# Performance work log

Measured on AMD Instinct MI355X. Metric: run time of the kernel, lower is better.

## Reference

```python
import jax, jax.numpy as jnp
import numpy as np

M = 2048            # input image is M x M
N_ANGLES = 64       # theta = [0, 1, ..., 63] radians (raw floats, as in the TF layer)

# Daubechies-like 2x2 filters, reshaped row-major exactly like tf.reshape([...,4],[2,2,1,1])
HIGH_F = jnp.array([[-0.1384, 0.7243], [-0.6038, 0.1601]], dtype=jnp.float32)


def setup_inputs() -> dict:
    key = jax.random.key(0)
    image = jax.random.normal(key, (M, M), dtype=jnp.float32)
    return {"image": image}


def _dwt_high(image):
    # tf.nn.conv2d(x, k, strides=2, padding='SAME') with single in/out channel.
    # Input dims are even so SAME adds no padding; out = (H/2, W/2).
    x = image[None, :, :, None]
    k = HIGH_F[:, :, None, None]  # HWIO
    y = jax.lax.conv_general_dilated(
        x, k, window_strides=(2, 2), padding='SAME',
        dimension_numbers=('NHWC', 'HWIO', 'NHWC'))
    return y[0, :, :, 0]


def _pad_square(img):
    # Static (trace-time) padding math, mirrors prepare_img.
    h, w = img.shape
    diagonal = np.sqrt(2) * max(h, w)
    pad = [int(np.ceil(diagonal - s)) for s in (h, w)]
    new_center = [(s + p) // 2 for s, p in zip((h, w), pad)]
    old_center = [s // 2 for s in (h, w)]
    pad_before = [nc - oc for oc, nc in zip(old_center, new_center)]
    pad_width = [(pb, p - pb) for pb, p in zip(pad_before, pad)]
    padded = jnp.pad(img, pad_width, mode='constant', constant_values=0.0)
    center = padded.shape[0] // 2
    return padded, center


def _rotate_sum(img, center, out_h, out_w, angle):
    # ImageProjectiveTransformV3 (BILINEAR, fill_mode=WRAP) followed by sum over rows.
    H, W = img.shape
    xs = jnp.arange(out_w, dtype=jnp.float32)
    ys = jnp.arange(out_h, dtype=jnp.float32)
    X, Y = jnp.meshgrid(xs, ys)  # [out_h, out_w]
    c, s = jnp.cos(angle), jnp.sin(angle)
    x_in = c * X + s * Y - center * (c + s - 1.0)
    y_in = -s * X + c * Y - center * (c - s - 1.0)
    x0 = jnp.floor(x_in)
    y0 = jnp.floor(y_in)
    dx = x_in - x0
    dy = y_in - y0
    # WRAP fill mode: periodic wrapping of sample indices
    x0i = jnp.mod(x0.astype(jnp.int32), W)
    x1i = jnp.mod(x0i + 1, W)
    y0i = jnp.mod(y0.astype(jnp.int32), H)
    y1i = jnp.mod(y0i + 1, H)
    v00 = img[y0i, x0i]
    v01 = img[y0i, x1i]
    v10 = img[y1i, x0i]
    v11 = img[y1i, x1i]
    rotated = (v00 * (1 - dy) * (1 - dx) + v01 * (1 - dy) * dx
               + v10 * dy * (1 - dx) + v11 * dy * dx)
    return rotated.sum(axis=0)  # column sums -> one radon line, length out_w


def reference(image):
    theta = jnp.arange(N_ANGLES, dtype=jnp.float32)  # radians, matches init theta
    high = _dwt_high(image)                          # (1024, 1024)
    padded, center = _pad_square(high)               # (1449, 1449), center 724
    out_h, out_w = padded.shape[0] - 1, padded.shape[1] - 1
    lines = jax.vmap(lambda a: _rotate_sum(padded, center, out_h, out_w, a))(theta)
    A = lines.T                                      # (out_w, n_angles)
    return A / jnp.max(A)
```

## Files before the change

kernel.cpp:

```cpp
#include <hip/hip_runtime.h>
#include <hip/hip_bf16.h>
#include <hip/hip_fp16.h>


#define HM 1024
#define PW 1449
#define PWS 1450
#define PAD0 212
#define OW 1448
#define NA 64
#define NOUT (OW * NA)
#define CENTER 724.0f
#define XS_N 181
#define YS 4
#define NWAVES (XS_N * NA * YS)
#define NBLOCKS (NWAVES / 4)
#define NRP ((size_t)PW * PWS)
#define NPAD ((size_t)PW * PW)

#ifndef __has_builtin
#define __has_builtin(x) 0
#endif
#if __has_builtin(__builtin_amdgcn_fdot2) && __has_builtin(__builtin_amdgcn_cvt_pkrtz)
#define USE_DOT2 1
typedef _Float16 h2 __attribute__((ext_vector_type(2)));
__device__ __forceinline__ h2 pkrtz(float a, float b) {
    return __builtin_bit_cast(h2, __builtin_amdgcn_cvt_pkrtz(a, b));
}
#else
#define USE_DOT2 0
#endif

__device__ __forceinline__ float conv_at(const float* __restrict__ img, int r, int c) {
    int i = r - PAD0;
    int j = c - PAD0;
    if ((unsigned)i >= (unsigned)HM || (unsigned)j >= (unsigned)HM) return 0.0f;
    const float2* r0 = reinterpret_cast<const float2*>(img + (size_t)(2 * i) * 2048);
    const float2* r1 = reinterpret_cast<const float2*>(img + (size_t)(2 * i + 1) * 2048);
    float2 a = r0[j];
    float2 b = r1[j];
    return fmaf(-0.1384f, a.x,
           fmaf( 0.7243f, a.y,
           fmaf(-0.6038f, b.x, 0.1601f * b.y)));
}

__global__ __launch_bounds__(256) void k_pack(const float* __restrict__ img,
                                              unsigned int* __restrict__ RP) {
    int gid = blockIdx.x * blockDim.x + threadIdx.x;
    if (gid >= (int)NRP) return;
    int r = gid / PWS;
    int x = gid - r * PWS;
    int cx = (x == PW) ? 0 : x;
    int r1 = (r == PW - 1) ? 0 : r + 1;
    float v0 = conv_at(img, r, cx);
    float v1 = conv_at(img, r1, cx);
    __half2 h = __floats2half2_rn(v0, v1);
    RP[gid] = *reinterpret_cast<unsigned int*>(&h);
}

__device__ __forceinline__ float blend4(uint2 q, float dx, float dy, float acc) {
#if USE_DOT2
    float omdx = 1.0f - dx;
    float omdy = 1.0f - dy;
    h2 w0 = pkrtz(omdy * omdx, dy * omdx);
    h2 w1 = pkrtz(omdy * dx,   dy * dx);
    acc = __builtin_amdgcn_fdot2(__builtin_bit_cast(h2, q.x), w0, acc, false);
    acc = __builtin_amdgcn_fdot2(__builtin_bit_cast(h2, q.y), w1, acc, false);
    return acc;
#else
    float2 f0 = __half22float2(*reinterpret_cast<const __half2*>(&q.x));
    float2 f1 = __half22float2(*reinterpret_cast<const __half2*>(&q.y));
    float top = fmaf(dx, f1.x - f0.x, f0.x);
    float bot = fmaf(dx, f1.y - f0.y, f0.y);
    return fmaf(dy, bot - top, acc + top);
#endif
}

__device__ __forceinline__ float blend4_val(uint2 q, float dx, float dy) {
#if USE_DOT2
    float omdx = 1.0f - dx;
    float omdy = 1.0f - dy;
    h2 w0 = pkrtz(omdy * omdx, dy * omdx);
    h2 w1 = pkrtz(omdy * dx,   dy * dx);
    float t = __builtin_amdgcn_fdot2(__builtin_bit_cast(h2, q.x), w0, 0.0f, false);
    return __builtin_amdgcn_fdot2(__builtin_bit_cast(h2, q.y), w1, t, false);
#else
    float2 f0 = __half22float2(*reinterpret_cast<const __half2*>(&q.x));
    float2 f1 = __half22float2(*reinterpret_cast<const __half2*>(&q.y));
    float top = fmaf(dx, f1.x - f0.x, f0.x);
    float bot = fmaf(dx, f1.y - f0.y, f0.y);
    return fmaf(dy, bot - top, top);
#endif
}

__global__ __launch_bounds__(256) void k_proj5(const unsigned int* __restrict__ RP,
                                               float* __restrict__ partial) {
    int wave_id = blockIdx.x * 4 + (threadIdx.x >> 6);
    int lane = threadIdx.x & 63;
    int lx = lane & 7;
    int ly = lane >> 3;

    int xs = wave_id % XS_N;
    int t  = wave_id / XS_N;
    int a  = t & (NA - 1);
    int chunk = t >> 6;

    int X0 = xs * 8;
    int X = X0 + lx;

    float fa = (float)a;
    float c = cosf(fa);
    float s = sinf(fa);
    float bx = -CENTER * (c + s - 1.0f);
    float by = -CENTER * (c - s - 1.0f);
    float cx0 = fmaf(c, (float)X, bx);
    float cy0 = fmaf(-s, (float)X, by);
    float cxs = cx0 + (float)PW;
    float cys = cy0 + (float)PW;

    int oct_beg = (chunk * XS_N) / YS;
    int oct_end = ((chunk + 1) * XS_N) / YS;
    int noct = oct_end - oct_beg;

    float ab = fabsf(c) + fabsf(s);
    float E = fmaf(3.5f, ab, 2.0f);
    float D = 3.5f * ab;
    float xcw = fmaf(c, (float)X0 + 3.5f, bx);
    float ycw = fmaf(-s, (float)X0 + 3.5f, by);
    float ycen = (float)((oct_beg + lane) * 8) + 3.5f;
    float xcf = fmaf(s, ycen, xcw);
    float ycf = fmaf(c, ycen, ycw);
    float uxf = xcf - 211.0f + E + 1449.0f;
    float uyf = ycf - 211.0f + E + 1449.0f;
    unsigned iux = (unsigned)uxf;
    unsigned iuy = (unsigned)uyf;
    unsigned mxr = iux - __umul24(__umul24(iux, 11581u) >> 24, 1449u);
    unsigned myr = iuy - __umul24(__umul24(iuy, 11581u) >> 24, 1449u);
    unsigned lim = (unsigned)(1026.0f + 2.0f * E);
    bool act = (lane < noct) && (mxr <= lim) && (myr <= lim);
    bool interior = (xcf - D >= 213.0f) && (xcf + D <= 1234.0f) &&
                    (ycf - D >= 213.0f) && (ycf + D <= 1234.0f);
    unsigned long long mask_int  = __ballot(act && interior);
    unsigned long long mask_edge = __ballot(act && !interior);

    float fly = (float)ly;
    float acc = 0.0f;

    while (mask_int) {
        int tb = (int)__builtin_ctzll(mask_int);
        mask_int &= mask_int - 1;
        float yb = (float)((oct_beg + tb) << 3);
        float yf = yb + fly;
        float x_in = fmaf(s, yf, cx0);
        float y_in = fmaf(c, yf, cy0);
        int ix = (int)x_in;
        int iy = (int)y_in;
        float dx = x_in - (float)ix;
        float dy = y_in - (float)iy;
        unsigned idx = __umul24((unsigned)iy, PWS) + (unsigned)ix;
        uint2 q = *reinterpret_cast<const uint2*>(RP + idx);
        acc = blend4(q, dx, dy, acc);
    }

    while (mask_edge) {
        int tb = (int)__builtin_ctzll(mask_edge);
        mask_edge &= mask_edge - 1;
        float yb = (float)((oct_beg + tb) << 3);
        float yf = yb + fly;
        float x_s = fmaf(s, yf, cxs);
        float y_s = fmaf(c, yf, cys);
        int ixs = (int)x_s;
        int iys = (int)y_s;
        float dx = x_s - (float)ixs;
        float dy = y_s - (float)iys;
        unsigned vx = (unsigned)ixs;
        unsigned vy = (unsigned)iys;
        unsigned x0 = vx - __umul24(__umul24(vx, 11581u) >> 24, 1449u);
        unsigned y0 = vy - __umul24(__umul24(vy, 11581u) >> 24, 1449u);
        bool ok = ((x0 - (PAD0 - 1)) <= 1024u) && ((y0 - (PAD0 - 1)) <= 1024u);
        unsigned idx = __umul24(y0, PWS) + x0;
        uint2 q = *reinterpret_cast<const uint2*>(RP + idx);
        float contrib = blend4_val(q, dx, dy);
        acc += ok ? contrib : 0.0f;
    }

    acc += __shfl_xor(acc, 8, 64);
    acc += __shfl_xor(acc, 16, 64);
    acc += __shfl_xor(acc, 32, 64);

    if (ly == 0) partial[(size_t)chunk * NOUT + a * OW + X] = acc;
}

__global__ __launch_bounds__(256) void k_pad_dwt(const float* __restrict__ img,
                                                 float* __restrict__ P) {
    int gid = blockIdx.x * blockDim.x + threadIdx.x;
    if (gid >= PW * PW) return;
    int r = gid / PW;
    int cidx = gid - r * PW;
    P[gid] = conv_at(img, r, cidx);
}

__global__ __launch_bounds__(256) void k_proj3(const float* __restrict__ P,
                                               float* __restrict__ partial) {
    int wave_id = blockIdx.x * 4 + (threadIdx.x >> 6);
    int lane = threadIdx.x & 63;
    int lx = lane & 7;
    int ly = lane >> 3;

    int xs = wave_id % XS_N;
    int t  = wave_id / XS_N;
    int a  = t & (NA - 1);
    int chunk = t >> 6;

    int X0 = xs * 8;
    int X = X0 + lx;

    float fa = (float)a;
    float c = cosf(fa);
    float s = sinf(fa);
    float bx = -CENTER * (c + s - 1.0f);
    float by = -CENTER * (c - s - 1.0f);
    float cxs = fmaf(c, (float)X, bx) + (float)PW;
    float cys = fmaf(-s, (float)X, by) + (float)PW;

    int oct_beg = (chunk * XS_N) / YS;
    int oct_end = ((chunk + 1) * XS_N) / YS;
    int noct = oct_end - oct_beg;

    float E = fmaf(3.5f, fabsf(c) + fabsf(s), 2.0f);
    float xcw = fmaf(c, (float)X0 + 3.5f, bx);
    float ycw = fmaf(-s, (float)X0 + 3.5f, by);
    float ycen = (float)((oct_beg + lane) * 8) + 3.5f;
    float uxf = fmaf(s, ycen, xcw) - 211.0f + E + 1449.0f;
    float uyf = fmaf(c, ycen, ycw) - 211.0f + E + 1449.0f;
    unsigned iux = (unsigned)uxf;
    unsigned iuy = (unsigned)uyf;
    unsigned mxr = iux - ((iux * 11581u) >> 24) * 1449u;
    unsigned myr = iuy - ((iuy * 11581u) >> 24) * 1449u;
    unsigned lim = (unsigned)(1026.0f + 2.0f * E);
    bool act = (lane < noct) && (mxr <= lim) && (myr <= lim);
    unsigned long long mask = __ballot(act);

    float acc = 0.0f;
    while (mask) {
        int tb = (int)__builtin_ctzll(mask);
        mask &= mask - 1;
        float yf = (float)(((oct_beg + tb) << 3) + ly);
        float x_s = fmaf(s, yf, cxs);
        float y_s = fmaf(c, yf, cys);
        float fx = floorf(x_s);
        float fy = floorf(y_s);
        float dx = x_s - fx;
        float dy = y_s - fy;
        unsigned vx = (unsigned)fx;
        unsigned vy = (unsigned)fy;
        int x0 = (int)(vx - ((vx * 11581u) >> 24) * 1449u);
        int y0 = (int)(vy - ((vy * 11581u) >> 24) * 1449u);
        bool ok = ((unsigned)(x0 - (PAD0 - 1)) <= 1024u) &&
                  ((unsigned)(y0 - (PAD0 - 1)) <= 1024u);
        const float* p0 = P + (y0 * PW + x0);
        float2 tv = *reinterpret_cast<const float2*>(p0);
        float2 bv = *reinterpret_cast<const float2*>(p0 + PW);
        float top = fmaf(dx, tv.y - tv.x, tv.x);
        float bot = fmaf(dx, bv.y - bv.x, bv.x);
        float contrib = fmaf(dy, bot - top, top);
        acc += ok ? contrib : 0.0f;
    }

    acc += __shfl_xor(acc, 8, 64);
    acc += __shfl_xor(acc, 16, 64);
    acc += __shfl_xor(acc, 32, 64);

    if (ly == 0) partial[(size_t)chunk * NOUT + a * OW + X] = acc;
}

template <int NCH>
__global__ __launch_bounds__(256) void k_combine(const float* __restrict__ partial,
                                                 float* __restrict__ out) {
    int gid = blockIdx.x * blockDim.x + threadIdx.x;
    if (gid >= NOUT) return;
    float sum = 0.0f;
#pragma unroll
    for (int cth = 0; cth < NCH; ++cth) sum += partial[(size_t)cth * NOUT + gid];
    int a = gid / OW;
    int x = gid % OW;
    out[x * NA + a] = sum;
}

__global__ __launch_bounds__(256) void k_max1(const float* __restrict__ out,
                                              float* __restrict__ bmax) {
    __shared__ float sm[4];
    const float4* o4 = reinterpret_cast<const float4*>(out);
    const int n4 = NOUT / 4;
    float m = -3.4e38f;
    for (int i = blockIdx.x * 256 + threadIdx.x; i < n4; i += gridDim.x * 256) {
        float4 v = o4[i];
        m = fmaxf(fmaxf(fmaxf(m, v.x), fmaxf(v.y, v.z)), v.w);
    }
#pragma unroll
    for (int off = 32; off > 0; off >>= 1) m = fmaxf(m, __shfl_down(m, off, 64));
    int lane = threadIdx.x & 63;
    int w = threadIdx.x >> 6;
    if (lane == 0) sm[w] = m;
    __syncthreads();
    if (threadIdx.x == 0)
        bmax[blockIdx.x] = fmaxf(fmaxf(sm[0], sm[1]), fmaxf(sm[2], sm[3]));
}

__global__ __launch_bounds__(64) void k_max2(const float* __restrict__ bmax,
                                             float* __restrict__ mx) {
    float m = bmax[threadIdx.x];
#pragma unroll
    for (int off = 32; off > 0; off >>= 1) m = fmaxf(m, __shfl_down(m, off, 64));
    if (threadIdx.x == 0) *mx = m;
}

__global__ __launch_bounds__(256) void k_norm(float* __restrict__ out,
                                              const float* __restrict__ mx) {
    int gid = blockIdx.x * blockDim.x + threadIdx.x;
    if (gid < NOUT) out[gid] = out[gid] / (*mx);
}

extern "C" void kernel_launch(void* const* d_in, const int* in_sizes, int n_in,
                              void* d_out, int out_size, void* d_ws, size_t ws_size,
                              hipStream_t stream) {
    const float* img = (const float*)d_in[0];
    float* out = (float*)d_out;

    const size_t need_new = (NRP + 16) * 4 + ((size_t)YS * NOUT + 65) * 4;
    const size_t np_alloc = NPAD + PW + 8;
    const size_t need_old = np_alloc * 4 + ((size_t)YS * NOUT + 65) * 4;

    if (ws_size >= need_new) {
        unsigned int* RP = (unsigned int*)d_ws;
        float* partial = (float*)(RP + NRP + 16);
        float* bmax = partial + (size_t)YS * NOUT;
        float* mx = bmax + 64;
        k_pack<<<(int)((NRP + 255) / 256), 256, 0, stream>>>(img, RP);
        k_proj5<<<NBLOCKS, 256, 0, stream>>>(RP, partial);
        k_combine<YS><<<(NOUT + 255) / 256, 256, 0, stream>>>(partial, out);
        k_max1<<<64, 256, 0, stream>>>(out, bmax);
        k_max2<<<1, 64, 0, stream>>>(bmax, mx);
        k_norm<<<(NOUT + 255) / 256, 256, 0, stream>>>(out, mx);
    } else if (ws_size >= need_old) {
        float* P = (float*)d_ws;
        float* partial = P + np_alloc;
        float* bmax = partial + (size_t)YS * NOUT;
        float* mx = bmax + 64;
        k_pad_dwt<<<(int)((NPAD + 255) / 256), 256, 0, stream>>>(img, P);
        k_proj3<<<NBLOCKS, 256, 0, stream>>>(P, partial);
        k_combine<YS><<<(NOUT + 255) / 256, 256, 0, stream>>>(partial, out);
        k_max1<<<64, 256, 0, stream>>>(out, bmax);
        k_max2<<<1, 64, 0, stream>>>(bmax, mx);
        k_norm<<<(NOUT + 255) / 256, 256, 0, stream>>>(out, mx);
    }
}
```

Before: 90.74 us.

## Fuse combine with block max, pack four rows per thread, precompute trig

Three changes. The partial-sum combine now also computes per-block maxima, so the separate max pass that re-read the output is gone. The packing kernel handles four rows per thread, so each DWT row is evaluated once instead of twice across neighbouring row pairs. Per-angle cos/sin come from a tiny precomputed table instead of being recomputed in every wave. This adds one extra small launch (k_trig), and the second max stage now reduces 362 block maxima.

```diff
diff --git a/kernel.cpp b/kernel.cpp
--- a/kernel.cpp
+++ b/kernel.cpp
@@ -17,6 +17,7 @@
 #define NBLOCKS (NWAVES / 4)
 #define NRP ((size_t)PW * PWS)
 #define NPAD ((size_t)PW * PW)
+#define NQ 363
 
 #ifndef __has_builtin
 #define __has_builtin(x) 0
@@ -44,18 +45,36 @@
            fmaf(-0.6038f, b.x, 0.1601f * b.y)));
 }
 
-__global__ __launch_bounds__(256) void k_pack(const float* __restrict__ img,
-                                              unsigned int* __restrict__ RP) {
+__global__ __launch_bounds__(64) void k_trig(float2* __restrict__ cs) {
+    int i = threadIdx.x;
+    cs[i] = make_float2(cosf((float)i), sinf((float)i));
+}
+
+__global__ __launch_bounds__(256) void k_pack4(const float* __restrict__ img,
+                                               unsigned int* __restrict__ RP) {
     int gid = blockIdx.x * blockDim.x + threadIdx.x;
-    if (gid >= (int)NRP) return;
-    int r = gid / PWS;
-    int x = gid - r * PWS;
-    int cx = (x == PW) ? 0 : x;
-    int r1 = (r == PW - 1) ? 0 : r + 1;
-    float v0 = conv_at(img, r, cx);
-    float v1 = conv_at(img, r1, cx);
-    __half2 h = __floats2half2_rn(v0, v1);
-    RP[gid] = *reinterpret_cast<unsigned int*>(&h);
+    if (gid >= NQ * PWS) return;
+    int rq = gid / PWS;
+    int c = gid - rq * PWS;
+    int cx = (c == PW) ? 0 : c;
+    int r0 = rq * 4;
+    int nr = (PW - r0 < 4) ? (PW - r0) : 4;
+    float v[5];
+#pragma unroll
+    for (int k = 0; k <= 4; ++k) {
+        if (k <= nr) {
+            int row = r0 + k;
+            if (row == PW) row = 0;
+            v[k] = conv_at(img, row, cx);
+        }
+    }
+#pragma unroll
+    for (int k = 0; k < 4; ++k) {
+        if (k < nr) {
+            __half2 h = __floats2half2_rn(v[k], v[k + 1]);
+            RP[(size_t)(r0 + k) * PWS + c] = *reinterpret_cast<unsigned int*>(&h);
+        }
+    }
 }
 
 __device__ __forceinline__ float blend4(uint2 q, float dx, float dy, float acc) {
@@ -93,8 +112,9 @@
 #endif
 }
 
-__global__ __launch_bounds__(256) void k_proj5(const unsigned int* __restrict__ RP,
-                                               float* __restrict__ partial) {
+__global__ __launch_bounds__(256) void k_proj5t(const unsigned int* __restrict__ RP,
+                                                const float2* __restrict__ cs,
+                                                float* __restrict__ partial) {
     int wave_id = blockIdx.x * 4 + (threadIdx.x >> 6);
     int lane = threadIdx.x & 63;
     int lx = lane & 7;
@@ -108,9 +128,9 @@
     int X0 = xs * 8;
     int X = X0 + lx;
 
-    float fa = (float)a;
-    float c = cosf(fa);
-    float s = sinf(fa);
+    float2 sc = cs[a];
+    float c = sc.x;
+    float s = sc.y;
     float bx = -CENTER * (c + s - 1.0f);
     float by = -CENTER * (c - s - 1.0f);
     float cx0 = fmaf(c, (float)X, bx);
@@ -189,6 +209,49 @@
     acc += __shfl_xor(acc, 32, 64);
 
     if (ly == 0) partial[(size_t)chunk * NOUT + a * OW + X] = acc;
+}
+
+__global__ __launch_bounds__(256) void k_combmax(const float* __restrict__ partial,
+                                                 float* __restrict__ out,
+                                                 float* __restrict__ bmax) {
+    __shared__ float sm[4];
+    int gid = blockIdx.x * 256 + threadIdx.x;
+    float sum = 0.0f;
+#pragma unroll
+    for (int cth = 0; cth < YS; ++cth) sum += partial[(size_t)cth * NOUT + gid];
+    int a = gid / OW;
+    int x = gid - a * OW;
+    out[x * NA + a] = sum;
+    float m = sum;
+#pragma unroll
+    for (int off = 32; off > 0; off >>= 1) m = fmaxf(m, __shfl_down(m, off, 64));
+    int lane = threadIdx.x & 63;
+    int w = threadIdx.x >> 6;
+    if (lane == 0) sm[w] = m;
+    __syncthreads();
+    if (threadIdx.x == 0)
+        bmax[blockIdx.x] = fmaxf(fmaxf(sm[0], sm[1]), fmaxf(sm[2], sm[3]));
+}
+
+__global__ __launch_bounds__(256) void k_max2(const float* __restrict__ bmax,
+                                              float* __restrict__ mx) {
+    __shared__ float sm[4];
+    float m = -3.4e38f;
+    for (int i = threadIdx.x; i < 362; i += 256) m = fmaxf(m, bmax[i]);
+#pragma unroll
+    for (int off = 32; off > 0; off >>= 1) m = fmaxf(m, __shfl_down(m, off, 64));
+    int lane = threadIdx.x & 63;
+    int w = threadIdx.x >> 6;
+    if (lane == 0) sm[w] = m;
+    __syncthreads();
+    if (threadIdx.x == 0)
+        *mx = fmaxf(fmaxf(sm[0], sm[1]), fmaxf(sm[2], sm[3]));
+}
+
+__global__ __launch_bounds__(256) void k_norm(float* __restrict__ out,
+                                              const float* __restrict__ mx) {
+    int gid = blockIdx.x * blockDim.x + threadIdx.x;
+    if (gid < NOUT) out[gid] = out[gid] / (*mx);
 }
 
 __global__ __launch_bounds__(256) void k_pad_dwt(const float* __restrict__ img,
@@ -274,84 +337,37 @@
     if (ly == 0) partial[(size_t)chunk * NOUT + a * OW + X] = acc;
 }
 
-template <int NCH>
-__global__ __launch_bounds__(256) void k_combine(const float* __restrict__ partial,
-                                                 float* __restrict__ out) {
-    int gid = blockIdx.x * blockDim.x + threadIdx.x;
-    if (gid >= NOUT) return;
-    float sum = 0.0f;
-#pragma unroll
-    for (int cth = 0; cth < NCH; ++cth) sum += partial[(size_t)cth * NOUT + gid];
-    int a = gid / OW;
-    int x = gid % OW;
-    out[x * NA + a] = sum;
-}
-
-__global__ __launch_bounds__(256) void k_max1(const float* __restrict__ out,
-                                              float* __restrict__ bmax) {
-    __shared__ float sm[4];
-    const float4* o4 = reinterpret_cast<const float4*>(out);
-    const int n4 = NOUT / 4;
-    float m = -3.4e38f;
-    for (int i = blockIdx.x * 256 + threadIdx.x; i < n4; i += gridDim.x * 256) {
-        float4 v = o4[i];
-        m = fmaxf(fmaxf(fmaxf(m, v.x), fmaxf(v.y, v.z)), v.w);
-    }
-#pragma unroll
-    for (int off = 32; off > 0; off >>= 1) m = fmaxf(m, __shfl_down(m, off, 64));
-    int lane = threadIdx.x & 63;
-    int w = threadIdx.x >> 6;
-    if (lane == 0) sm[w] = m;
-    __syncthreads();
-    if (threadIdx.x == 0)
-        bmax[blockIdx.x] = fmaxf(fmaxf(sm[0], sm[1]), fmaxf(sm[2], sm[3]));
-}
-
-__global__ __launch_bounds__(64) void k_max2(const float* __restrict__ bmax,
-                                             float* __restrict__ mx) {
-    float m = bmax[threadIdx.x];
-#pragma unroll
-    for (int off = 32; off > 0; off >>= 1) m = fmaxf(m, __shfl_down(m, off, 64));
-    if (threadIdx.x == 0) *mx = m;
-}
-
-__global__ __launch_bounds__(256) void k_norm(float* __restrict__ out,
-                                              const float* __restrict__ mx) {
-    int gid = blockIdx.x * blockDim.x + threadIdx.x;
-    if (gid < NOUT) out[gid] = out[gid] / (*mx);
-}
-
 extern "C" void kernel_launch(void* const* d_in, const int* in_sizes, int n_in,
                               void* d_out, int out_size, void* d_ws, size_t ws_size,
                               hipStream_t stream) {
     const float* img = (const float*)d_in[0];
     float* out = (float*)d_out;
 
-    const size_t need_new = (NRP + 16) * 4 + ((size_t)YS * NOUT + 65) * 4;
+    const size_t need_new = (NRP + 16) * 4 + ((size_t)YS * NOUT + 512 + 1 + 128) * 4;
     const size_t np_alloc = NPAD + PW + 8;
-    const size_t need_old = np_alloc * 4 + ((size_t)YS * NOUT + 65) * 4;
+    const size_t need_old = np_alloc * 4 + ((size_t)YS * NOUT + 512 + 1) * 4;
 
     if (ws_size >= need_new) {
         unsigned int* RP = (unsigned int*)d_ws;
         float* partial = (float*)(RP + NRP + 16);
         float* bmax = partial + (size_t)YS * NOUT;
-        float* mx = bmax + 64;
-        k_pack<<<(int)((NRP + 255) / 256), 256, 0, stream>>>(img, RP);
-        k_proj5<<<NBLOCKS, 256, 0, stream>>>(RP, partial);
-        k_combine<YS><<<(NOUT + 255) / 256, 256, 0, stream>>>(partial, out);
-        k_max1<<<64, 256, 0, stream>>>(out, bmax);
-        k_max2<<<1, 64, 0, stream>>>(bmax, mx);
+        float* mx = bmax + 512;
+        float2* cs = (float2*)(mx + 1);
+        k_trig<<<1, 64, 0, stream>>>(cs);
+        k_pack4<<<(NQ * PWS + 255) / 256, 256, 0, stream>>>(img, RP);
+        k_proj5t<<<NBLOCKS, 256, 0, stream>>>(RP, cs, partial);
+        k_combmax<<<NOUT / 256, 256, 0, stream>>>(partial, out, bmax);
+        k_max2<<<1, 256, 0, stream>>>(bmax, mx);
         k_norm<<<(NOUT + 255) / 256, 256, 0, stream>>>(out, mx);
     } else if (ws_size >= need_old) {
         float* P = (float*)d_ws;
         float* partial = P + np_alloc;
         float* bmax = partial + (size_t)YS * NOUT;
-        float* mx = bmax + 64;
+        float* mx = bmax + 512;
         k_pad_dwt<<<(int)((NPAD + 255) / 256), 256, 0, stream>>>(img, P);
         k_proj3<<<NBLOCKS, 256, 0, stream>>>(P, partial);
-        k_combine<YS><<<(NOUT + 255) / 256, 256, 0, stream>>>(partial, out);
-        k_max1<<<64, 256, 0, stream>>>(out, bmax);
-        k_max2<<<1, 64, 0, stream>>>(bmax, mx);
+        k_combmax<<<NOUT / 256, 256, 0, stream>>>(partial, out, bmax);
+        k_max2<<<1, 256, 0, stream>>>(bmax, mx);
         k_norm<<<(NOUT + 255) / 256, 256, 0, stream>>>(out, mx);
     }
 }
```

Result: slower. 94.36 us (+4.0%).
